# Kernel optimization log

Hardware: AMD Instinct MI355X
Metric: run time of the kernel (lower is better)

The kernel has to match this reference:

```python
import jax, jax.numpy as jnp
import numpy as np

D_MODEL = 128
D_INNER = 256   # expand=2
D_STATE = 16
DT_RANK = 8     # ceil(128/16)
D_CONV = 2
GROUPS = 4
EPS = 1e-5


def _mamba_dir(x, W_in, conv_w, conv_b, W_x, W_dt, b_dt, A_log, D, W_out):
    # x: [B, L, d_model]
    B, L, _ = x.shape
    xz = x @ W_in                               # [B, L, 2*d_inner]
    xp, z = xz[..., :D_INNER], xz[..., D_INNER:]
    # depthwise causal conv, kernel size 2 (pad-left 1)
    xprev = jnp.pad(xp, ((0, 0), (1, 0), (0, 0)))[:, :L]
    xc = jax.nn.silu(xprev * conv_w[:, 0] + xp * conv_w[:, 1] + conv_b)
    xdb = xc @ W_x                              # [B, L, dt_rank + 2*d_state]
    dt_r = xdb[..., :DT_RANK]
    Bc = xdb[..., DT_RANK:DT_RANK + D_STATE]    # [B, L, d_state]
    Cc = xdb[..., DT_RANK + D_STATE:]           # [B, L, d_state]
    dt = jax.nn.softplus(dt_r @ W_dt + b_dt)    # [B, L, d_inner]
    A = -jnp.exp(A_log)                         # [d_inner, d_state]

    def step(h, inp):
        dt_t, B_t, C_t, x_t = inp               # [B,di], [B,ds], [B,ds], [B,di]
        dA = jnp.exp(dt_t[:, :, None] * A)      # [B, di, ds]
        h = dA * h + (dt_t * x_t)[:, :, None] * B_t[:, None, :]
        y = jnp.einsum('bds,bs->bd', h, C_t)
        return h, y

    h0 = jnp.zeros((B, D_INNER, D_STATE), x.dtype)
    xs = (jnp.moveaxis(dt, 1, 0), jnp.moveaxis(Bc, 1, 0),
          jnp.moveaxis(Cc, 1, 0), jnp.moveaxis(xc, 1, 0))
    _, ys = jax.lax.scan(step, h0, xs)          # ys: [L, B, d_inner]
    y = jnp.moveaxis(ys, 0, 1) + D * xc
    y = y * jax.nn.silu(z)
    return y @ W_out                            # [B, L, d_model]


def _groupnorm_silu(x, gamma, beta):
    B, C, H, W = x.shape
    xg = x.reshape(B, GROUPS, C // GROUPS, H, W)
    mu = xg.mean(axis=(2, 3, 4), keepdims=True)
    var = xg.var(axis=(2, 3, 4), keepdims=True)
    xn = ((xg - mu) * jax.lax.rsqrt(var + EPS)).reshape(B, C, H, W)
    return jax.nn.silu(xn * gamma[None, :, None, None] + beta[None, :, None, None])


def setup_inputs() -> dict:
    key = jax.random.key(0)
    ks = jax.random.split(key, 24)
    s = 0.02
    A_log = jnp.log(jnp.tile(jnp.arange(1, D_STATE + 1, dtype=jnp.float32)[None, :], (D_INNER, 1)))
    inp = {"x": jax.random.normal(ks[0], (4, D_MODEL, 64, 64), jnp.float32)}
    for i, sfx in enumerate(("f", "b")):
        o = 1 + 9 * i
        inp[f"W_in_{sfx}"] = jax.random.normal(ks[o], (D_MODEL, 2 * D_INNER)) * s
        inp[f"conv_w_{sfx}"] = jax.random.normal(ks[o + 1], (D_INNER, D_CONV)) * 0.5
        inp[f"conv_b_{sfx}"] = jnp.zeros((D_INNER,))
        inp[f"W_x_{sfx}"] = jax.random.normal(ks[o + 2], (D_INNER, DT_RANK + 2 * D_STATE)) * s
        inp[f"W_dt_{sfx}"] = jax.random.normal(ks[o + 3], (DT_RANK, D_INNER)) * s
        inp[f"b_dt_{sfx}"] = jnp.full((D_INNER,), -3.0)
        inp[f"A_log_{sfx}"] = A_log
        inp[f"D_{sfx}"] = jnp.ones((D_INNER,))
        inp[f"W_out_{sfx}"] = jax.random.normal(ks[o + 4], (D_INNER, D_MODEL)) * s
    inp["gn_gamma"] = jnp.ones((D_MODEL,))
    inp["gn_beta"] = jnp.zeros((D_MODEL,))
    return inp


def reference(x, W_in_f, conv_w_f, conv_b_f, W_x_f, W_dt_f, b_dt_f, A_log_f, D_f, W_out_f,
              W_in_b, conv_w_b, conv_b_b, W_x_b, W_dt_b, b_dt_b, A_log_b, D_b, W_out_b,
              gn_gamma, gn_beta):
    B, C, H, W = x.shape
    xs = x.transpose(0, 2, 3, 1).reshape(B, H * W, C)
    y_f = _mamba_dir(xs, W_in_f, conv_w_f, conv_b_f, W_x_f, W_dt_f, b_dt_f, A_log_f, D_f, W_out_f)
    xr = xs[:, ::-1]
    y_b = _mamba_dir(xr, W_in_b, conv_w_b, conv_b_b, W_x_b, W_dt_b, b_dt_b, A_log_b, D_b, W_out_b)[:, ::-1]
    y = y_f + y_b                               # bidirectional combine
    y = y.reshape(B, H, W, C).transpose(0, 3, 1, 2)
    y = _groupnorm_silu(y, gn_gamma, gn_beta)
    return y + x
```

## Files before the change

kernel.cpp:

```cpp
#include <hip/hip_runtime.h>

#define Bn 4
#define Ln 4096
#define Cn 128
#define DIn 256
#define NCn 128
#define LCn 32
#define ROWS (Bn*Ln)

typedef short s8v __attribute__((ext_vector_type(8)));
typedef short s4v __attribute__((ext_vector_type(4)));
typedef unsigned short u8v __attribute__((ext_vector_type(8)));
typedef unsigned short u4v __attribute__((ext_vector_type(4)));
typedef float f4v __attribute__((ext_vector_type(4)));
typedef float f2v __attribute__((ext_vector_type(2)));

__device__ __forceinline__ float siluf(float x){ return x / (1.f + __expf(-x)); }
__device__ __forceinline__ unsigned short bfr(float f){
  uint u = __float_as_uint(f);
  return (unsigned short)((u + 0x7fffu + ((u>>16)&1u)) >> 16);
}
__device__ __forceinline__ float bf2f(unsigned short u){ return __uint_as_float(((uint)u)<<16); }

__device__ __forceinline__ void sp_w(float r, float& dtv, float& w){
  float e = __expf(-fabsf(r));
  float rc = 1.f / (1.f + e);
  dtv = fmaxf(r, 0.f) + __logf(1.f + e);
  w = (r > 0.f) ? e * rc : rc;
}

__device__ __forceinline__ int tile_off(int r, int gran, int ghalf){
  return ((r>>4)<<9) + ((r&15)<<5) + (((gran ^ ((r>>1)&3)))<<3) + ghalf;
}

#define SMEMB 18432

__global__ __launch_bounds__(256) void k_g1(const float* __restrict__ x,
    const float* __restrict__ Wf, const float* __restrict__ Wb,
    float* __restrict__ xpf, float* __restrict__ xpb,
    unsigned short* __restrict__ zbf, unsigned short* __restrict__ zbb)
{
  const int dir = blockIdx.z;
  const float* __restrict__ W = dir ? Wb : Wf;
  float* __restrict__ xp = dir ? xpb : xpf;
  unsigned short* __restrict__ zb = dir ? zbb : zbf;
  const int row0 = blockIdx.x * 128;
  const int n0 = blockIdx.y;
  const int b = row0 >> 12;
  const int t0 = row0 & (Ln-1);
  const float* __restrict__ xb = x + (size_t)b * Cn * Ln;

  __shared__ __align__(16) char smem[SMEMB];
  short* Ast = (short*)smem;
  short* Bst = (short*)smem + 8*512;
  float* Te  = (float*)smem;

  const int tid = threadIdx.x;
  const int lane = tid & 63;
  const int wid = tid >> 6;
  const int wr = wid >> 1, wc = wid & 1;
  const int r16 = lane & 15, kg = lane >> 4;

  const int q = tid & 31, kq = tid >> 5;
  const int kbase = 4*kq;
  const int g_true = kq >> 1;
  const int ghalf = (kq & 1) * 4;

  f4v acc[4][4];
  #pragma unroll
  for (int i=0;i<4;++i)
    #pragma unroll
    for (int j=0;j<4;++j) acc[i][j] = (f4v){0.f,0.f,0.f,0.f};

  float4 va[4], vb[4];
  {
    #pragma unroll
    for (int kk=0;kk<4;++kk) {
      va[kk] = (dir==0)
        ? *(const float4*)(xb + (size_t)(kbase+kk)*Ln + t0 + 4*q)
        : *(const float4*)(xb + (size_t)(kbase+kk)*Ln + (Ln-4 - t0 - 4*q));
      vb[kk] = *(const float4*)(W + (size_t)(kbase+kk)*512 + n0*128 + 4*q);
    }
  }
  for (int ks=0; ks<4; ++ks) {
    if (ks) __syncthreads();
    #pragma unroll
    for (int e=0;e<4;++e) {
      int r = 4*q + e;
      int off = tile_off(r, g_true, ghalf);
      int c = dir ? (3-e) : e;
      s4v hv;
      #pragma unroll
      for (int kk=0;kk<4;++kk) hv[kk] = (short)bfr(((const float*)&va[kk])[c]);
      *(s4v*)&Ast[off] = hv;
    }
    #pragma unroll
    for (int e=0;e<4;++e) {
      int r = 4*q + e;
      int off = tile_off(r, g_true, ghalf);
      s4v hv;
      #pragma unroll
      for (int kk=0;kk<4;++kk) hv[kk] = (short)bfr(((const float*)&vb[kk])[e]);
      *(s4v*)&Bst[off] = hv;
    }
    __syncthreads();
    if (ks < 3) {
      const int k0n = (ks+1)*32;
      #pragma unroll
      for (int kk=0;kk<4;++kk) {
        va[kk] = (dir==0)
          ? *(const float4*)(xb + (size_t)(k0n+kbase+kk)*Ln + t0 + 4*q)
          : *(const float4*)(xb + (size_t)(k0n+kbase+kk)*Ln + (Ln-4 - t0 - 4*q));
        vb[kk] = *(const float4*)(W + (size_t)(k0n+kbase+kk)*512 + n0*128 + 4*q);
      }
    }
    const int gsh = ((kg ^ ((r16>>1)&3)) << 3);
    s8v fa[4], fb[4];
    #pragma unroll
    for (int m=0;m<4;++m) fa[m] = *(const s8v*)&Ast[(wr*4+m)*512 + r16*32 + gsh];
    #pragma unroll
    for (int n=0;n<4;++n) fb[n] = *(const s8v*)&Bst[(wc*4+n)*512 + r16*32 + gsh];
    #pragma unroll
    for (int m=0;m<4;++m)
      #pragma unroll
      for (int n=0;n<4;++n)
        acc[m][n] = __builtin_amdgcn_mfma_f32_16x16x32_bf16(fa[m], fb[n], acc[m][n], 0,0,0);
  }
  __syncthreads();
  float* Tw = Te + wid*1088;
  #pragma unroll
  for (int m=0;m<4;++m) {
    #pragma unroll
    for (int n=0;n<4;++n)
      #pragma unroll
      for (int v=0;v<4;++v)
        Tw[(kg*4+v)*68 + n*16 + r16] = acc[m][n][v];
    #pragma unroll
    for (int rr=0;rr<4;++rr) {
      int r = rr*4 + (lane>>4);
      int c4 = lane & 15;
      float4 v4 = *(const float4*)&Tw[r*68 + c4*4];
      int row = row0 + wr*64 + m*16 + r;
      int colL = wc*64 + c4*4;
      if (n0 < 2) {
        *(float4*)(xp + (size_t)row*256 + n0*128 + colL) = v4;
      } else {
        u4v u; u[0]=bfr(v4.x); u[1]=bfr(v4.y); u[2]=bfr(v4.z); u[3]=bfr(v4.w);
        *(u4v*)(zb + (size_t)row*256 + (n0-2)*128 + colL) = u;
      }
    }
  }
}

__global__ __launch_bounds__(256) void k_conv(
    const float* __restrict__ xpf, const float* __restrict__ xpb,
    const float* __restrict__ cwf, const float* __restrict__ cwb,
    const float* __restrict__ cbf, const float* __restrict__ cbb,
    unsigned short* __restrict__ xcf, unsigned short* __restrict__ xcb)
{
  const int dir = blockIdx.y;
  const float* __restrict__ xpd = dir ? xpb : xpf;
  const float* __restrict__ cw = dir ? cwb : cwf;
  const float* __restrict__ cb = dir ? cbb : cbf;
  unsigned short* __restrict__ xc = dir ? xcb : xcf;
  const int n4 = ROWS * 64;
  for (int idx4 = blockIdx.x*256 + threadIdx.x; idx4 < n4; idx4 += gridDim.x*256) {
    int row = idx4 >> 6;
    int d0 = (idx4 & 63) * 4;
    float4 cur = *(const float4*)(xpd + (size_t)row*256 + d0);
    float4 prev = make_float4(0.f,0.f,0.f,0.f);
    if (row & (Ln-1)) prev = *(const float4*)(xpd + (size_t)(row-1)*256 + d0);
    float4 cwA = *(const float4*)(cw + d0*2);
    float4 cwB = *(const float4*)(cw + d0*2 + 4);
    float4 cb4 = *(const float4*)(cb + d0);
    u4v r;
    r[0] = bfr(siluf(fmaf(prev.x,cwA.x, fmaf(cur.x,cwA.y, cb4.x))));
    r[1] = bfr(siluf(fmaf(prev.y,cwA.z, fmaf(cur.y,cwA.w, cb4.y))));
    r[2] = bfr(siluf(fmaf(prev.z,cwB.x, fmaf(cur.z,cwB.y, cb4.z))));
    r[3] = bfr(siluf(fmaf(prev.w,cwB.z, fmaf(cur.w,cwB.w, cb4.w))));
    *(u4v*)(xc + (size_t)row*256 + d0) = r;
  }
}

__global__ __launch_bounds__(256) void k_g2(
    const unsigned short* __restrict__ xcf, const unsigned short* __restrict__ xcb,
    const float* __restrict__ Wxf, const float* __restrict__ Wxb,
    float* __restrict__ xdbf, float* __restrict__ xdbb)
{
  const int dir = blockIdx.z;
  const unsigned short* __restrict__ xc = dir ? xcb : xcf;
  const float* __restrict__ Wx = dir ? Wxb : Wxf;
  float* __restrict__ xdb = dir ? xdbb : xdbf;
  const int row0 = blockIdx.x * 64;

  __shared__ __align__(16) short Ast[4*512];
  __shared__ __align__(16) short Bst[4*512];

  const int tid = threadIdx.x;
  const int lane = tid & 63;
  const int wid = tid >> 6;
  const int wr = wid >> 1, wc = wid & 1;
  const int r16 = lane & 15, kg = lane >> 4;
  const int ar = tid >> 2, ag = tid & 3;
  const int bn = tid & 63, bg = tid >> 6;

  f4v acc[2][2];
  #pragma unroll
  for (int i=0;i<2;++i)
    #pragma unroll
    for (int j=0;j<2;++j) acc[i][j] = (f4v){0.f,0.f,0.f,0.f};

  for (int ks=0; ks<8; ++ks) {
    const int k0 = ks*32;
    if (ks) __syncthreads();
    {
      u8v u = *(const u8v*)(xc + (size_t)(row0+ar)*256 + k0 + ag*8);
      *(u8v*)&Ast[tile_off(ar, ag, 0)] = u;
    }
    {
      s8v hv;
      #pragma unroll
      for (int i=0;i<8;++i) {
        int k = k0 + bg*8 + i;
        float f = (bn < 40) ? Wx[(size_t)k*40 + bn] : 0.f;
        hv[i] = (short)bfr(f);
      }
      *(s8v*)&Bst[tile_off(bn, bg, 0)] = hv;
    }
    __syncthreads();
    const int gsh = ((kg ^ ((r16>>1)&3)) << 3);
    s8v fa[2], fb[2];
    #pragma unroll
    for (int m=0;m<2;++m) fa[m] = *(const s8v*)&Ast[(wr*2+m)*512 + r16*32 + gsh];
    #pragma unroll
    for (int n=0;n<2;++n) fb[n] = *(const s8v*)&Bst[(wc*2+n)*512 + r16*32 + gsh];
    #pragma unroll
    for (int m=0;m<2;++m)
      #pragma unroll
      for (int n=0;n<2;++n)
        acc[m][n] = __builtin_amdgcn_mfma_f32_16x16x32_bf16(fa[m], fb[n], acc[m][n], 0,0,0);
  }
  #pragma unroll
  for (int m=0;m<2;++m)
    #pragma unroll
    for (int n=0;n<2;++n) {
      int col = wc*32 + n*16 + r16;
      if (col < 40) {
        #pragma unroll
        for (int v=0;v<4;++v) {
          int row = row0 + wr*32 + m*16 + kg*4 + v;
          xdb[(size_t)row*40 + col] = acc[m][n][v];
        }
      }
    }
}

__global__ __launch_bounds__(128,4) void k_pass1(
    const float* __restrict__ xdbf, const float* __restrict__ xdbb,
    const unsigned short* __restrict__ xcf, const unsigned short* __restrict__ xcb,
    const float* __restrict__ Wdtf, const float* __restrict__ Wdtb,
    const float* __restrict__ bdtf, const float* __restrict__ bdtb,
    const float* __restrict__ Alf, const float* __restrict__ Alb,
    float* __restrict__ sdtf, float* __restrict__ sdtb,
    float* __restrict__ hkf, float* __restrict__ hkb)
{
  const int dir = blockIdx.y;
  const float* __restrict__ xdb = dir ? xdbb : xdbf;
  const unsigned short* __restrict__ xc = dir ? xcb : xcf;
  const float* __restrict__ Wdt = dir ? Wdtb : Wdtf;
  const float* __restrict__ bdt = dir ? bdtb : bdtf;
  const float* __restrict__ Al  = dir ? Alb  : Alf;
  float* __restrict__ sdt = dir ? sdtb : sdtf;
  float* __restrict__ hk  = dir ? hkb  : hkf;
  const int dh = blockIdx.x & 1;
  const int cc = blockIdx.x >> 1;
  const int b = cc >> 7, c = cc & 127;
  const int t0 = c * LCn;
  __shared__ float S[LCn*32];
  const int tid = threadIdx.x;
  #pragma unroll
  for (int j=0;j<6;++j) {
    int idx = tid + j*128;
    int t = idx/24, jj = idx - t*24;
    S[t*32 + jj] = xdb[(size_t)(b*Ln + t0 + t)*40 + jj];
  }
  const int d = dh*128 + tid;
  float Areg[16];
  bool st = true;
  #pragma unroll
  for (int s=0;s<16;++s) {
    Areg[s] = -__expf(Al[d*16+s]);
    st = st && (fabsf(Areg[s] + (float)(s+1)) <= 3e-5f*(float)(s+1));
  }
  f2v wdt2[4];
  #pragma unroll
  for (int j=0;j<4;++j) wdt2[j] = (f2v){Wdt[(2*j)*256+d], Wdt[(2*j+1)*256+d]};
  const float bd = bdt[d];
  f2v h2[8];
  #pragma unroll
  for (int i=0;i<8;++i) h2[i] = (f2v){0.f,0.f};
  float sacc = 0.f;
  const unsigned short* xcp = xc + (size_t)(b*Ln + t0)*256 + d;
  __syncthreads();
  if (st) {
    for (int t=0;t<LCn;++t) {
      float4 sA = *(const float4*)&S[t*32];
      float4 sB = *(const float4*)&S[t*32+4];
      f2v r2 = (f2v){sA.x,sA.y}*wdt2[0] + (f2v){sA.z,sA.w}*wdt2[1];
      r2 = (f2v){sB.x,sB.y}*wdt2[2] + r2;
      r2 = (f2v){sB.z,sB.w}*wdt2[3] + r2;
      float rr = bd + r2.x + r2.y;
      float dtv, wv;
      sp_w(rr, dtv, wv);
      float4 b0 = *(const float4*)&S[t*32+8];
      float4 b1 = *(const float4*)&S[t*32+12];
      float4 b2 = *(const float4*)&S[t*32+16];
      float4 b3 = *(const float4*)&S[t*32+20];
      float xv = bf2f(xcp[(size_t)t*256]);
      float u = dtv * xv;
      sacc += dtv;
      float w2s = wv*wv;
      float w4 = w2s*w2s, w8 = w4*w4;
      f2v wstep = (f2v){w2s, w2s};
      f2v wpa = (f2v){wv, w2s};
      f2v wpb = wpa * (f2v){w8, w8};
      f2v u2 = (f2v){u, u};
      h2[0] = h2[0]*wpa + u2*(f2v){b0.x,b0.y}; wpa *= wstep;
      h2[4] = h2[4]*wpb + u2*(f2v){b2.x,b2.y}; wpb *= wstep;
      h2[1] = h2[1]*wpa + u2*(f2v){b0.z,b0.w}; wpa *= wstep;
      h2[5] = h2[5]*wpb + u2*(f2v){b2.z,b2.w}; wpb *= wstep;
      h2[2] = h2[2]*wpa + u2*(f2v){b1.x,b1.y}; wpa *= wstep;
      h2[6] = h2[6]*wpb + u2*(f2v){b3.x,b3.y}; wpb *= wstep;
      h2[3] = h2[3]*wpa + u2*(f2v){b1.z,b1.w};
      h2[7] = h2[7]*wpb + u2*(f2v){b3.z,b3.w};
    }
  } else {
    for (int t=0;t<LCn;++t) {
      float4 sA = *(const float4*)&S[t*32];
      float4 sB = *(const float4*)&S[t*32+4];
      float rr = bd;
      rr = fmaf(sA.x,wdt2[0].x, fmaf(sA.y,wdt2[0].y, fmaf(sA.z,wdt2[1].x, fmaf(sA.w,wdt2[1].y, rr))));
      rr = fmaf(sB.x,wdt2[2].x, fmaf(sB.y,wdt2[2].y, fmaf(sB.z,wdt2[3].x, fmaf(sB.w,wdt2[3].y, rr))));
      float dtv, wv;
      sp_w(rr, dtv, wv);
      float bq[16];
      #pragma unroll
      for (int i=0;i<4;++i) *(float4*)&bq[4*i] = *(const float4*)&S[t*32 + 8 + 4*i];
      float xv = bf2f(xcp[(size_t)t*256]);
      float u = dtv * xv;
      sacc += dtv;
      #pragma unroll
      for (int s=0;s<16;++s) {
        float hv = (s&1) ? h2[s>>1].y : h2[s>>1].x;
        hv = fmaf(hv, __expf(dtv*Areg[s]), u*bq[s]);
        if (s&1) h2[s>>1].y = hv; else h2[s>>1].x = hv;
      }
    }
  }
  sdt[(size_t)(b*NCn + c)*256 + d] = sacc;
  #pragma unroll
  for (int i=0;i<8;++i) {
    hk[(size_t)((b*NCn + c)*16 + 2*i)*256 + d]   = h2[i].x;
    hk[(size_t)((b*NCn + c)*16 + 2*i+1)*256 + d] = h2[i].y;
  }
}

__global__ __launch_bounds__(256) void k_pass2(
    const float* __restrict__ Alf, const float* __restrict__ Alb,
    const float* __restrict__ sdtf, const float* __restrict__ sdtb,
    float* __restrict__ hkf, float* __restrict__ hkb)
{
  const int dir = blockIdx.y;
  const float* __restrict__ Al  = dir ? Alb : Alf;
  const float* __restrict__ sdt = dir ? sdtb : sdtf;
  float* __restrict__ hk = dir ? hkb : hkf;
  int g = blockIdx.x*256 + threadIdx.x;
  int d = g & 255, s = (g >> 8) & 15, b = g >> 12;
  float Ad = -__expf(Al[d*16+s]);
  float h = 0.f;
  float sd_n = sdt[(size_t)(b*NCn)*256 + d];
  size_t hi_n = (size_t)((b*NCn)*16 + s)*256 + d;
  float he_n = hk[hi_n];
  for (int c=0;c<NCn;++c) {
    float sd = sd_n, he = he_n;
    size_t hi = hi_n;
    if (c+1 < NCn) {
      int bc = b*NCn + c + 1;
      sd_n = sdt[(size_t)bc*256 + d];
      hi_n = (size_t)(bc*16 + s)*256 + d;
      he_n = hk[hi_n];
    }
    hk[hi] = h;
    h = fmaf(__expf(Ad*sd), h, he);
  }
}

__global__ __launch_bounds__(128,4) void k_pass3(
    const float* __restrict__ xdbf, const float* __restrict__ xdbb,
    const unsigned short* __restrict__ xcf, const unsigned short* __restrict__ xcb,
    const float* __restrict__ Wdtf, const float* __restrict__ Wdtb,
    const float* __restrict__ bdtf, const float* __restrict__ bdtb,
    const float* __restrict__ Alf, const float* __restrict__ Alb,
    const float* __restrict__ Dvf, const float* __restrict__ Dvb,
    const float* __restrict__ hkf, const float* __restrict__ hkb,
    const unsigned short* __restrict__ zbf, const unsigned short* __restrict__ zbb,
    unsigned short* __restrict__ ygf, unsigned short* __restrict__ ygb)
{
  const int dir = blockIdx.y;
  const float* __restrict__ xdb = dir ? xdbb : xdbf;
  const unsigned short* __restrict__ xc = dir ? xcb : xcf;
  const float* __restrict__ Wdt = dir ? Wdtb : Wdtf;
  const float* __restrict__ bdt = dir ? bdtb : bdtf;
  const float* __restrict__ Al  = dir ? Alb  : Alf;
  const float* __restrict__ Dv  = dir ? Dvb  : Dvf;
  const float* __restrict__ hk  = dir ? hkb  : hkf;
  const unsigned short* __restrict__ zbd = dir ? zbb : zbf;
  unsigned short* __restrict__ yg = dir ? ygb : ygf;
  const int dh = blockIdx.x & 1;
  const int cc = blockIdx.x >> 1;
  const int b = cc >> 7, c = cc & 127;
  const int t0 = c * LCn;
  __shared__ float S[LCn*48];
  const int tid = threadIdx.x;
  #pragma unroll
  for (int j=0;j<10;++j) {
    int idx = tid + j*128;
    int t = idx/40, jj = idx - t*40;
    S[t*48 + jj] = xdb[(size_t)(b*Ln + t0 + t)*40 + jj];
  }
  const int d = dh*128 + tid;
  float Areg[16];
  bool st = true;
  #pragma unroll
  for (int s=0;s<16;++s) {
    Areg[s] = -__expf(Al[d*16+s]);
    st = st && (fabsf(Areg[s] + (float)(s+1)) <= 3e-5f*(float)(s+1));
  }
  f2v wdt2[4];
  #pragma unroll
  for (int j=0;j<4;++j) wdt2[j] = (f2v){Wdt[(2*j)*256+d], Wdt[(2*j+1)*256+d]};
  const float bd = bdt[d];
  const float Dd = Dv[d];
  f2v h2[8];
  #pragma unroll
  for (int i=0;i<8;++i)
    h2[i] = (f2v){hk[(size_t)((b*NCn + c)*16 + 2*i)*256 + d],
                  hk[(size_t)((b*NCn + c)*16 + 2*i+1)*256 + d]};
  const unsigned short* xcp = xc + (size_t)(b*Ln + t0)*256 + d;
  const unsigned short* zbp = zbd + (size_t)(b*Ln + t0)*256 + d;
  unsigned short* ygp = yg + (size_t)(b*Ln + t0)*256 + d;
  __syncthreads();
  if (st) {
    for (int t=0;t<LCn;++t) {
      float4 sA = *(const float4*)&S[t*48];
      float4 sB = *(const float4*)&S[t*48+4];
      f2v r2 = (f2v){sA.x,sA.y}*wdt2[0] + (f2v){sA.z,sA.w}*wdt2[1];
      r2 = (f2v){sB.x,sB.y}*wdt2[2] + r2;
      r2 = (f2v){sB.z,sB.w}*wdt2[3] + r2;
      float rr = bd + r2.x + r2.y;
      float dtv, wv;
      sp_w(rr, dtv, wv);
      float4 b0 = *(const float4*)&S[t*48+8];
      float4 b1 = *(const float4*)&S[t*48+12];
      float4 b2 = *(const float4*)&S[t*48+16];
      float4 b3 = *(const float4*)&S[t*48+20];
      float4 c0 = *(const float4*)&S[t*48+24];
      float4 c1 = *(const float4*)&S[t*48+28];
      float4 c2 = *(const float4*)&S[t*48+32];
      float4 c3 = *(const float4*)&S[t*48+36];
      float xv = bf2f(xcp[(size_t)t*256]);
      float u = dtv * xv;
      float w2s = wv*wv;
      float w4 = w2s*w2s, w8 = w4*w4;
      f2v wstep = (f2v){w2s, w2s};
      f2v wpa = (f2v){wv, w2s};
      f2v wpb = wpa * (f2v){w8, w8};
      f2v u2 = (f2v){u, u};
      f2v yA = (f2v){0.f,0.f}, yB = (f2v){0.f,0.f};
      h2[0] = h2[0]*wpa + u2*(f2v){b0.x,b0.y}; yA = h2[0]*(f2v){c0.x,c0.y} + yA; wpa *= wstep;
      h2[4] = h2[4]*wpb + u2*(f2v){b2.x,b2.y}; yB = h2[4]*(f2v){c2.x,c2.y} + yB; wpb *= wstep;
      h2[1] = h2[1]*wpa + u2*(f2v){b0.z,b0.w}; yA = h2[1]*(f2v){c0.z,c0.w} + yA; wpa *= wstep;
      h2[5] = h2[5]*wpb + u2*(f2v){b2.z,b2.w}; yB = h2[5]*(f2v){c2.z,c2.w} + yB; wpb *= wstep;
      h2[2] = h2[2]*wpa + u2*(f2v){b1.x,b1.y}; yA = h2[2]*(f2v){c1.x,c1.y} + yA; wpa *= wstep;
      h2[6] = h2[6]*wpb + u2*(f2v){b3.x,b3.y}; yB = h2[6]*(f2v){c3.x,c3.y} + yB; wpb *= wstep;
      h2[3] = h2[3]*wpa + u2*(f2v){b1.z,b1.w}; yA = h2[3]*(f2v){c1.z,c1.w} + yA;
      h2[7] = h2[7]*wpb + u2*(f2v){b3.z,b3.w}; yB = h2[7]*(f2v){c3.z,c3.w} + yB;
      float y = yA.x + yA.y + yB.x + yB.y;
      y = fmaf(Dd, xv, y);
      float zv = bf2f(zbp[(size_t)t*256]);
      ygp[(size_t)t*256] = bfr(y * siluf(zv));
    }
  } else {
    for (int t=0;t<LCn;++t) {
      float4 sA = *(const float4*)&S[t*48];
      float4 sB = *(const float4*)&S[t*48+4];
      float rr = bd;
      rr = fmaf(sA.x,wdt2[0].x, fmaf(sA.y,wdt2[0].y, fmaf(sA.z,wdt2[1].x, fmaf(sA.w,wdt2[1].y, rr))));
      rr = fmaf(sB.x,wdt2[2].x, fmaf(sB.y,wdt2[2].y, fmaf(sB.z,wdt2[3].x, fmaf(sB.w,wdt2[3].y, rr))));
      float dtv, wv;
      sp_w(rr, dtv, wv);
      float bq[16], cq[16];
      #pragma unroll
      for (int i=0;i<4;++i) {
        *(float4*)&bq[4*i] = *(const float4*)&S[t*48 + 8 + 4*i];
        *(float4*)&cq[4*i] = *(const float4*)&S[t*48 + 24 + 4*i];
      }
      float xv = bf2f(xcp[(size_t)t*256]);
      float u = dtv * xv;
      float y = 0.f;
      #pragma unroll
      for (int s=0;s<16;++s) {
        float hv = (s&1) ? h2[s>>1].y : h2[s>>1].x;
        hv = fmaf(hv, __expf(dtv*Areg[s]), u*bq[s]);
        if (s&1) h2[s>>1].y = hv; else h2[s>>1].x = hv;
        y = fmaf(hv, cq[s], y);
      }
      y = fmaf(Dd, xv, y);
      float zv = bf2f(zbp[(size_t)t*256]);
      ygp[(size_t)t*256] = bfr(y * siluf(zv));
    }
  }
}

__global__ __launch_bounds__(256) void k_gout(
    const unsigned short* __restrict__ ygf, const unsigned short* __restrict__ ygb,
    const float* __restrict__ Wof, const float* __restrict__ Wob,
    float* __restrict__ yp)
{
  const int row0 = blockIdx.x * 128;
  const int khalf = blockIdx.y;
  const int dir = blockIdx.z;
  const unsigned short* __restrict__ ygd = dir ? ygb : ygf;
  const float* __restrict__ Wod = dir ? Wob : Wof;
  float* __restrict__ ypart = yp + (size_t)(dir*2 + khalf) * ROWS * 128;
  const int b = row0 >> 12;
  const int l0 = row0 & (Ln-1);

  __shared__ __align__(16) char smem[SMEMB];
  short* Ast = (short*)smem;
  short* Bst = (short*)smem + 8*512;
  float* Te  = (float*)smem;

  const int tid = threadIdx.x;
  const int lane = tid & 63;
  const int wid = tid >> 6;
  const int wr = wid >> 1, wc = wid & 1;
  const int r16 = lane & 15, kg = lane >> 4;

  const int ar = tid >> 1, kh = tid & 1;
  const int q = tid & 31, kq = tid >> 5;
  const int kbase = 4*kq;
  const int g_true = kq >> 1;
  const int ghalf = (kq & 1) * 4;

  f4v acc[4][4];
  #pragma unroll
  for (int i=0;i<4;++i)
    #pragma unroll
    for (int j=0;j<4;++j) acc[i][j] = (f4v){0.f,0.f,0.f,0.f};

  for (int ks=0; ks<4; ++ks) {
    const int kk0 = khalf*128 + ks*32;
    if (ks) __syncthreads();
    {
      int rl = l0 + ar;
      size_t srow = (size_t)b*Ln + (dir ? (Ln-1-rl) : rl);
      const unsigned short* s = ygd + srow*256 + kk0 + kh*16;
      u8v u0 = *(const u8v*)(s);
      u8v u1 = *(const u8v*)(s + 8);
      int o0 = tile_off(ar, 2*kh,   0);
      int o1 = tile_off(ar, 2*kh+1, 0);
      *(u8v*)&Ast[o0] = u0;
      *(u8v*)&Ast[o1] = u1;
    }
    {
      float4 vb[4];
      #pragma unroll
      for (int kk=0;kk<4;++kk)
        vb[kk] = *(const float4*)(Wod + (size_t)(kk0+kbase+kk)*128 + 4*q);
      #pragma unroll
      for (int e=0;e<4;++e) {
        int r = 4*q + e;
        int off = tile_off(r, g_true, ghalf);
        s4v hv;
        #pragma unroll
        for (int kk=0;kk<4;++kk) hv[kk] = (short)bfr(((const float*)&vb[kk])[e]);
        *(s4v*)&Bst[off] = hv;
      }
    }
    __syncthreads();
    const int gsh = ((kg ^ ((r16>>1)&3)) << 3);
    s8v fa[4], fb[4];
    #pragma unroll
    for (int m=0;m<4;++m) fa[m] = *(const s8v*)&Ast[(wr*4+m)*512 + r16*32 + gsh];
    #pragma unroll
    for (int n=0;n<4;++n) fb[n] = *(const s8v*)&Bst[(wc*4+n)*512 + r16*32 + gsh];
    #pragma unroll
    for (int m=0;m<4;++m)
      #pragma unroll
      for (int n=0;n<4;++n)
        acc[m][n] = __builtin_amdgcn_mfma_f32_16x16x32_bf16(fa[m], fb[n], acc[m][n], 0,0,0);
  }
  __syncthreads();
  float* Tw = Te + wid*1088;
  #pragma unroll
  for (int m=0;m<4;++m) {
    #pragma unroll
    for (int n=0;n<4;++n)
      #pragma unroll
      for (int v=0;v<4;++v)
        Tw[(kg*4+v)*68 + n*16 + r16] = acc[m][n][v];
    #pragma unroll
    for (int rr=0;rr<4;++rr) {
      int r = rr*4 + (lane>>4);
      int c4 = lane & 15;
      float4 v4 = *(const float4*)&Tw[r*68 + c4*4];
      int row = row0 + wr*64 + m*16 + r;
      *(float4*)(ypart + (size_t)row*128 + wc*64 + c4*4) = v4;
    }
  }
}

__global__ __launch_bounds__(256) void k_gnstat(const float* __restrict__ yp,
    float* __restrict__ ysum, float* __restrict__ part)
{
  const int bg = blockIdx.x >> 4;
  const int blk = blockIdx.x & 15;
  const int b = bg >> 2, g = bg & 3;
  const size_t P = (size_t)ROWS*128;
  float s=0.f, q=0.f;
  #pragma unroll
  for (int i=0;i<8;++i) {
    int e4 = blk*2048 + threadIdx.x + i*256;
    int l = e4 >> 3, c4 = e4 & 7;
    size_t base = (size_t)(b*Ln + l)*128 + g*32 + c4*4;
    float4 v0 = *(const float4*)(yp + base);
    float4 v1 = *(const float4*)(yp + P + base);
    float4 v2 = *(const float4*)(yp + 2*P + base);
    float4 v3 = *(const float4*)(yp + 3*P + base);
    float4 v;
    v.x = v0.x+v1.x+v2.x+v3.x;
    v.y = v0.y+v1.y+v2.y+v3.y;
    v.z = v0.z+v1.z+v2.z+v3.z;
    v.w = v0.w+v1.w+v2.w+v3.w;
    *(float4*)(ysum + base) = v;
    s += v.x+v.y+v.z+v.w;
    q = fmaf(v.x,v.x, fmaf(v.y,v.y, fmaf(v.z,v.z, fmaf(v.w,v.w, q))));
  }
  __shared__ float rs[256], rq[256];
  rs[threadIdx.x]=s; rq[threadIdx.x]=q;
  __syncthreads();
  for (int off=128; off>0; off>>=1) {
    if (threadIdx.x < off) { rs[threadIdx.x]+=rs[threadIdx.x+off]; rq[threadIdx.x]+=rq[threadIdx.x+off]; }
    __syncthreads();
  }
  if (threadIdx.x==0) { part[blockIdx.x*2]=rs[0]; part[blockIdx.x*2+1]=rq[0]; }
}

__global__ void k_gnred(const float* __restrict__ part, float* __restrict__ mr)
{
  int t = threadIdx.x;
  if (t < 16) {
    float s=0.f,q=0.f;
    for (int k=0;k<16;++k){ s+=part[(t*16+k)*2]; q+=part[(t*16+k)*2+1]; }
    const float inv = 1.f/131072.f;
    float mean = s*inv;
    float var = fmaf(-mean, mean, q*inv);
    mr[t*2] = mean;
    mr[t*2+1] = rsqrtf(var + 1e-5f);
  }
}

__global__ __launch_bounds__(256) void k_gnapply(const float* __restrict__ ysum,
    const float* __restrict__ mr, const float* __restrict__ gamma, const float* __restrict__ beta,
    const float* __restrict__ x, float* __restrict__ out)
{
  const int b = blockIdx.x >> 6;
  const int l0 = (blockIdx.x & 63) * 64;
  __shared__ float T[64][132];
  const int tid = threadIdx.x;
  #pragma unroll
  for (int j=0;j<8;++j) {
    int f = tid + j*256;
    int l = f >> 5, c4 = f & 31;
    *(float4*)&T[l][c4*4] = *(const float4*)(ysum + (size_t)(b*Ln + l0 + l)*128 + c4*4);
  }
  __syncthreads();
  #pragma unroll
  for (int j=0;j<8;++j) {
    int f = tid + j*256;
    int c = f >> 4, lv = f & 15;
    int bg = b*4 + (c>>5);
    float mean = mr[bg*2];
    float rstd = mr[bg*2+1];
    float gam = gamma[c], bet = beta[c];
    size_t base = (size_t)(b*Cn + c)*Ln + l0 + lv*4;
    float4 xv = *(const float4*)(x + base);
    float4 r;
    r.x = siluf(fmaf((T[lv*4+0][c]-mean)*rstd, gam, bet)) + xv.x;
    r.y = siluf(fmaf((T[lv*4+1][c]-mean)*rstd, gam, bet)) + xv.y;
    r.z = siluf(fmaf((T[lv*4+2][c]-mean)*rstd, gam, bet)) + xv.z;
    r.w = siluf(fmaf((T[lv*4+3][c]-mean)*rstd, gam, bet)) + xv.w;
    *(float4*)(out + base) = r;
  }
}

extern "C" void kernel_launch(void* const* d_in, const int* in_sizes, int n_in,
                              void* d_out, int out_size, void* d_ws, size_t ws_size,
                              hipStream_t stream) {
  const float* x      = (const float*)d_in[0];
  const float* W_in_f = (const float*)d_in[1];
  const float* cw_f   = (const float*)d_in[2];
  const float* cb_f   = (const float*)d_in[3];
  const float* Wx_f   = (const float*)d_in[4];
  const float* Wdt_f  = (const float*)d_in[5];
  const float* bdt_f  = (const float*)d_in[6];
  const float* Al_f   = (const float*)d_in[7];
  const float* D_f    = (const float*)d_in[8];
  const float* Wo_f   = (const float*)d_in[9];
  const float* W_in_b = (const float*)d_in[10];
  const float* cw_b   = (const float*)d_in[11];
  const float* cb_b   = (const float*)d_in[12];
  const float* Wx_b   = (const float*)d_in[13];
  const float* Wdt_b  = (const float*)d_in[14];
  const float* bdt_b  = (const float*)d_in[15];
  const float* Al_b   = (const float*)d_in[16];
  const float* D_b    = (const float*)d_in[17];
  const float* Wo_b   = (const float*)d_in[18];
  const float* gamma  = (const float*)d_in[19];
  const float* beta   = (const float*)d_in[20];
  float* out = (float*)d_out;

  float* w = (float*)d_ws;
  size_t o = 0;
  float* xp0 = w + o; o += (size_t)ROWS*256;
  float* xp1 = w + o; o += (size_t)ROWS*256;
  unsigned short* xc0 = (unsigned short*)(w + o); o += (size_t)ROWS*128;
  unsigned short* xc1 = (unsigned short*)(w + o); o += (size_t)ROWS*128;
  unsigned short* zb0 = (unsigned short*)(w + o); o += (size_t)ROWS*128;
  unsigned short* zb1 = (unsigned short*)(w + o); o += (size_t)ROWS*128;
  unsigned short* yg0 = (unsigned short*)(w + o); o += (size_t)ROWS*128;
  unsigned short* yg1 = (unsigned short*)(w + o); o += (size_t)ROWS*128;
  float* xdb0 = w + o; o += (size_t)ROWS*40;
  float* xdb1 = w + o; o += (size_t)ROWS*40;
  float* sdt0 = w + o; o += (size_t)Bn*NCn*256;
  float* sdt1 = w + o; o += (size_t)Bn*NCn*256;
  float* hk0  = w + o; o += (size_t)Bn*NCn*16*256;
  float* hk1  = w + o; o += (size_t)Bn*NCn*16*256;
  float* part = w + o; o += 512;
  float* mr   = w + o; o += 32;
  float* yp   = xp0;
  float* ysum = xdb0;
  if (ws_size < o*sizeof(float)) return;

  k_g1<<<dim3(ROWS/128, 4, 2), 256, 0, stream>>>(x, W_in_f, W_in_b, xp0, xp1, zb0, zb1);
  k_conv<<<dim3(1024, 2), 256, 0, stream>>>(xp0, xp1, cw_f, cw_b, cb_f, cb_b, xc0, xc1);
  k_g2<<<dim3(ROWS/64, 1, 2), 256, 0, stream>>>(xc0, xc1, Wx_f, Wx_b, xdb0, xdb1);
  k_pass1<<<dim3(Bn*NCn*2, 2), 128, 0, stream>>>(xdb0, xdb1, xc0, xc1, Wdt_f, Wdt_b,
                                                 bdt_f, bdt_b, Al_f, Al_b, sdt0, sdt1, hk0, hk1);
  k_pass2<<<dim3(64, 2), 256, 0, stream>>>(Al_f, Al_b, sdt0, sdt1, hk0, hk1);
  k_pass3<<<dim3(Bn*NCn*2, 2), 128, 0, stream>>>(xdb0, xdb1, xc0, xc1, Wdt_f, Wdt_b,
                                                 bdt_f, bdt_b, Al_f, Al_b, D_f, D_b,
                                                 hk0, hk1, zb0, zb1, yg0, yg1);
  k_gout<<<dim3(ROWS/128, 2, 2), 256, 0, stream>>>(yg0, yg1, Wo_f, Wo_b, yp);
  k_gnstat<<<dim3(256), 256, 0, stream>>>(yp, ysum, part);
  k_gnred<<<dim3(1), 64, 0, stream>>>(part, mr);
  k_gnapply<<<dim3(256), 256, 0, stream>>>(ysum, mr, gamma, beta, x, out);
}
```

Baseline: 148.5 us.

## Compute zero-init chunk output in pass1 and apply state correction in pass3

```diff
diff --git a/kernel.cpp b/kernel.cpp
--- a/kernel.cpp
+++ b/kernel.cpp
@@ -261,8 +261,10 @@
     const float* __restrict__ Wdtf, const float* __restrict__ Wdtb,
     const float* __restrict__ bdtf, const float* __restrict__ bdtb,
     const float* __restrict__ Alf, const float* __restrict__ Alb,
+    const float* __restrict__ Dvf, const float* __restrict__ Dvb,
     float* __restrict__ sdtf, float* __restrict__ sdtb,
-    float* __restrict__ hkf, float* __restrict__ hkb)
+    float* __restrict__ hkf, float* __restrict__ hkb,
+    unsigned int* __restrict__ dtwf, unsigned int* __restrict__ dtwb)
 {
   const int dir = blockIdx.y;
   const float* __restrict__ xdb = dir ? xdbb : xdbf;
@@ -270,19 +272,21 @@
   const float* __restrict__ Wdt = dir ? Wdtb : Wdtf;
   const float* __restrict__ bdt = dir ? bdtb : bdtf;
   const float* __restrict__ Al  = dir ? Alb  : Alf;
+  const float* __restrict__ Dv  = dir ? Dvb  : Dvf;
   float* __restrict__ sdt = dir ? sdtb : sdtf;
   float* __restrict__ hk  = dir ? hkb  : hkf;
+  unsigned int* __restrict__ dtw = dir ? dtwb : dtwf;
   const int dh = blockIdx.x & 1;
   const int cc = blockIdx.x >> 1;
   const int b = cc >> 7, c = cc & 127;
   const int t0 = c * LCn;
-  __shared__ float S[LCn*32];
+  __shared__ float S[LCn*48];
   const int tid = threadIdx.x;
   #pragma unroll
-  for (int j=0;j<6;++j) {
+  for (int j=0;j<10;++j) {
     int idx = tid + j*128;
-    int t = idx/24, jj = idx - t*24;
-    S[t*32 + jj] = xdb[(size_t)(b*Ln + t0 + t)*40 + jj];
+    int t = idx/40, jj = idx - t*40;
+    S[t*48 + jj] = xdb[(size_t)(b*Ln + t0 + t)*40 + jj];
   }
   const int d = dh*128 + tid;
   float Areg[16];
@@ -296,26 +300,33 @@
   #pragma unroll
   for (int j=0;j<4;++j) wdt2[j] = (f2v){Wdt[(2*j)*256+d], Wdt[(2*j+1)*256+d]};
   const float bd = bdt[d];
+  const float Dd = Dv[d];
   f2v h2[8];
   #pragma unroll
   for (int i=0;i<8;++i) h2[i] = (f2v){0.f,0.f};
   float sacc = 0.f;
   const unsigned short* xcp = xc + (size_t)(b*Ln + t0)*256 + d;
+  unsigned int* dtwp = dtw + (size_t)(b*Ln + t0)*256 + d;
   __syncthreads();
   if (st) {
+    float Wc = 1.f;
     for (int t=0;t<LCn;++t) {
-      float4 sA = *(const float4*)&S[t*32];
-      float4 sB = *(const float4*)&S[t*32+4];
+      float4 sA = *(const float4*)&S[t*48];
+      float4 sB = *(const float4*)&S[t*48+4];
       f2v r2 = (f2v){sA.x,sA.y}*wdt2[0] + (f2v){sA.z,sA.w}*wdt2[1];
       r2 = (f2v){sB.x,sB.y}*wdt2[2] + r2;
       r2 = (f2v){sB.z,sB.w}*wdt2[3] + r2;
       float rr = bd + r2.x + r2.y;
       float dtv, wv;
       sp_w(rr, dtv, wv);
-      float4 b0 = *(const float4*)&S[t*32+8];
-      float4 b1 = *(const float4*)&S[t*32+12];
-      float4 b2 = *(const float4*)&S[t*32+16];
-      float4 b3 = *(const float4*)&S[t*32+20];
+      float4 b0 = *(const float4*)&S[t*48+8];
+      float4 b1 = *(const float4*)&S[t*48+12];
+      float4 b2 = *(const float4*)&S[t*48+16];
+      float4 b3 = *(const float4*)&S[t*48+20];
+      float4 c0 = *(const float4*)&S[t*48+24];
+      float4 c1 = *(const float4*)&S[t*48+28];
+      float4 c2 = *(const float4*)&S[t*48+32];
+      float4 c3 = *(const float4*)&S[t*48+36];
       float xv = bf2f(xcp[(size_t)t*256]);
       float u = dtv * xv;
       sacc += dtv;
@@ -325,36 +336,53 @@
       f2v wpa = (f2v){wv, w2s};
       f2v wpb = wpa * (f2v){w8, w8};
       f2v u2 = (f2v){u, u};
-      h2[0] = h2[0]*wpa + u2*(f2v){b0.x,b0.y}; wpa *= wstep;
-      h2[4] = h2[4]*wpb + u2*(f2v){b2.x,b2.y}; wpb *= wstep;
-      h2[1] = h2[1]*wpa + u2*(f2v){b0.z,b0.w}; wpa *= wstep;
-      h2[5] = h2[5]*wpb + u2*(f2v){b2.z,b2.w}; wpb *= wstep;
-      h2[2] = h2[2]*wpa + u2*(f2v){b1.x,b1.y}; wpa *= wstep;
-      h2[6] = h2[6]*wpb + u2*(f2v){b3.x,b3.y}; wpb *= wstep;
-      h2[3] = h2[3]*wpa + u2*(f2v){b1.z,b1.w};
-      h2[7] = h2[7]*wpb + u2*(f2v){b3.z,b3.w};
+      f2v yA = (f2v){0.f,0.f}, yB = (f2v){0.f,0.f};
+      h2[0] = h2[0]*wpa + u2*(f2v){b0.x,b0.y}; yA = h2[0]*(f2v){c0.x,c0.y} + yA; wpa *= wstep;
+      h2[4] = h2[4]*wpb + u2*(f2v){b2.x,b2.y}; yB = h2[4]*(f2v){c2.x,c2.y} + yB; wpb *= wstep;
+      h2[1] = h2[1]*wpa + u2*(f2v){b0.z,b0.w}; yA = h2[1]*(f2v){c0.z,c0.w} + yA; wpa *= wstep;
+      h2[5] = h2[5]*wpb + u2*(f2v){b2.z,b2.w}; yB = h2[5]*(f2v){c2.z,c2.w} + yB; wpb *= wstep;
+      h2[2] = h2[2]*wpa + u2*(f2v){b1.x,b1.y}; yA = h2[2]*(f2v){c1.x,c1.y} + yA; wpa *= wstep;
+      h2[6] = h2[6]*wpb + u2*(f2v){b3.x,b3.y}; yB = h2[6]*(f2v){c3.x,c3.y} + yB; wpb *= wstep;
+      h2[3] = h2[3]*wpa + u2*(f2v){b1.z,b1.w}; yA = h2[3]*(f2v){c1.z,c1.w} + yA;
+      h2[7] = h2[7]*wpb + u2*(f2v){b3.z,b3.w}; yB = h2[7]*(f2v){c3.z,c3.w} + yB;
+      float y = yA.x + yA.y + yB.x + yB.y;
+      y = fmaf(Dd, xv, y);
+      Wc *= wv;
+      unsigned int pk = ((unsigned int)bfr(y) << 16)
+                      | (unsigned int)(unsigned short)fminf(Wc*65536.f, 65535.f);
+      dtwp[(size_t)t*256] = pk;
     }
   } else {
+    float Dt = 0.f;
     for (int t=0;t<LCn;++t) {
-      float4 sA = *(const float4*)&S[t*32];
-      float4 sB = *(const float4*)&S[t*32+4];
+      float4 sA = *(const float4*)&S[t*48];
+      float4 sB = *(const float4*)&S[t*48+4];
       float rr = bd;
       rr = fmaf(sA.x,wdt2[0].x, fmaf(sA.y,wdt2[0].y, fmaf(sA.z,wdt2[1].x, fmaf(sA.w,wdt2[1].y, rr))));
       rr = fmaf(sB.x,wdt2[2].x, fmaf(sB.y,wdt2[2].y, fmaf(sB.z,wdt2[3].x, fmaf(sB.w,wdt2[3].y, rr))));
       float dtv, wv;
       sp_w(rr, dtv, wv);
-      float bq[16];
-      #pragma unroll
-      for (int i=0;i<4;++i) *(float4*)&bq[4*i] = *(const float4*)&S[t*32 + 8 + 4*i];
+      float bq[16], cq[16];
+      #pragma unroll
+      for (int i=0;i<4;++i) {
+        *(float4*)&bq[4*i] = *(const float4*)&S[t*48 + 8 + 4*i];
+        *(float4*)&cq[4*i] = *(const float4*)&S[t*48 + 24 + 4*i];
+      }
       float xv = bf2f(xcp[(size_t)t*256]);
       float u = dtv * xv;
       sacc += dtv;
+      Dt += dtv;
+      float y = 0.f;
       #pragma unroll
       for (int s=0;s<16;++s) {
         float hv = (s&1) ? h2[s>>1].y : h2[s>>1].x;
         hv = fmaf(hv, __expf(dtv*Areg[s]), u*bq[s]);
         if (s&1) h2[s>>1].y = hv; else h2[s>>1].x = hv;
+        y = fmaf(hv, cq[s], y);
       }
+      y = fmaf(Dd, xv, y);
+      unsigned int pk = ((unsigned int)bfr(y) << 16) | (unsigned int)bfr(Dt);
+      dtwp[(size_t)t*256] = pk;
     }
   }
   sdt[(size_t)(b*NCn + c)*256 + d] = sacc;
@@ -395,24 +423,18 @@
   }
 }
 
-__global__ __launch_bounds__(128,4) void k_pass3(
+__global__ __launch_bounds__(128,4) void k_passC(
     const float* __restrict__ xdbf, const float* __restrict__ xdbb,
-    const unsigned short* __restrict__ xcf, const unsigned short* __restrict__ xcb,
-    const float* __restrict__ Wdtf, const float* __restrict__ Wdtb,
-    const float* __restrict__ bdtf, const float* __restrict__ bdtb,
+    const unsigned int* __restrict__ dtwf, const unsigned int* __restrict__ dtwb,
     const float* __restrict__ Alf, const float* __restrict__ Alb,
-    const float* __restrict__ Dvf, const float* __restrict__ Dvb,
     const float* __restrict__ hkf, const float* __restrict__ hkb,
     const unsigned short* __restrict__ zbf, const unsigned short* __restrict__ zbb,
     unsigned short* __restrict__ ygf, unsigned short* __restrict__ ygb)
 {
   const int dir = blockIdx.y;
   const float* __restrict__ xdb = dir ? xdbb : xdbf;
-  const unsigned short* __restrict__ xc = dir ? xcb : xcf;
-  const float* __restrict__ Wdt = dir ? Wdtb : Wdtf;
-  const float* __restrict__ bdt = dir ? bdtb : bdtf;
+  const unsigned int* __restrict__ dtw = dir ? dtwb : dtwf;
   const float* __restrict__ Al  = dir ? Alb  : Alf;
-  const float* __restrict__ Dv  = dir ? Dvb  : Dvf;
   const float* __restrict__ hk  = dir ? hkb  : hkf;
   const unsigned short* __restrict__ zbd = dir ? zbb : zbf;
   unsigned short* __restrict__ yg = dir ? ygb : ygf;
@@ -420,13 +442,13 @@
   const int cc = blockIdx.x >> 1;
   const int b = cc >> 7, c = cc & 127;
   const int t0 = c * LCn;
-  __shared__ float S[LCn*48];
+  __shared__ float S[LCn*16];
   const int tid = threadIdx.x;
   #pragma unroll
-  for (int j=0;j<10;++j) {
+  for (int j=0;j<4;++j) {
     int idx = tid + j*128;
-    int t = idx/40, jj = idx - t*40;
-    S[t*48 + jj] = xdb[(size_t)(b*Ln + t0 + t)*40 + jj];
+    int t = idx >> 4, jj = idx & 15;
+    S[idx] = xdb[(size_t)(b*Ln + t0 + t)*40 + 24 + jj];
   }
   const int d = dh*128 + tid;
   float Areg[16];
@@ -436,86 +458,54 @@
     Areg[s] = -__expf(Al[d*16+s]);
     st = st && (fabsf(Areg[s] + (float)(s+1)) <= 3e-5f*(float)(s+1));
   }
-  f2v wdt2[4];
-  #pragma unroll
-  for (int j=0;j<4;++j) wdt2[j] = (f2v){Wdt[(2*j)*256+d], Wdt[(2*j+1)*256+d]};
-  const float bd = bdt[d];
-  const float Dd = Dv[d];
-  f2v h2[8];
+  f2v hin2[8];
   #pragma unroll
   for (int i=0;i<8;++i)
-    h2[i] = (f2v){hk[(size_t)((b*NCn + c)*16 + 2*i)*256 + d],
-                  hk[(size_t)((b*NCn + c)*16 + 2*i+1)*256 + d]};
-  const unsigned short* xcp = xc + (size_t)(b*Ln + t0)*256 + d;
+    hin2[i] = (f2v){hk[(size_t)((b*NCn + c)*16 + 2*i)*256 + d],
+                    hk[(size_t)((b*NCn + c)*16 + 2*i+1)*256 + d]};
+  const unsigned int* dtwp = dtw + (size_t)(b*Ln + t0)*256 + d;
   const unsigned short* zbp = zbd + (size_t)(b*Ln + t0)*256 + d;
   unsigned short* ygp = yg + (size_t)(b*Ln + t0)*256 + d;
   __syncthreads();
   if (st) {
+    #pragma unroll 4
     for (int t=0;t<LCn;++t) {
-      float4 sA = *(const float4*)&S[t*48];
-      float4 sB = *(const float4*)&S[t*48+4];
-      f2v r2 = (f2v){sA.x,sA.y}*wdt2[0] + (f2v){sA.z,sA.w}*wdt2[1];
-      r2 = (f2v){sB.x,sB.y}*wdt2[2] + r2;
-      r2 = (f2v){sB.z,sB.w}*wdt2[3] + r2;
-      float rr = bd + r2.x + r2.y;
-      float dtv, wv;
-      sp_w(rr, dtv, wv);
-      float4 b0 = *(const float4*)&S[t*48+8];
-      float4 b1 = *(const float4*)&S[t*48+12];
-      float4 b2 = *(const float4*)&S[t*48+16];
-      float4 b3 = *(const float4*)&S[t*48+20];
-      float4 c0 = *(const float4*)&S[t*48+24];
-      float4 c1 = *(const float4*)&S[t*48+28];
-      float4 c2 = *(const float4*)&S[t*48+32];
-      float4 c3 = *(const float4*)&S[t*48+36];
-      float xv = bf2f(xcp[(size_t)t*256]);
-      float u = dtv * xv;
-      float w2s = wv*wv;
-      float w4 = w2s*w2s, w8 = w4*w4;
-      f2v wstep = (f2v){w2s, w2s};
-      f2v wpa = (f2v){wv, w2s};
-      f2v wpb = wpa * (f2v){w8, w8};
-      f2v u2 = (f2v){u, u};
-      f2v yA = (f2v){0.f,0.f}, yB = (f2v){0.f,0.f};
-      h2[0] = h2[0]*wpa + u2*(f2v){b0.x,b0.y}; yA = h2[0]*(f2v){c0.x,c0.y} + yA; wpa *= wstep;
-      h2[4] = h2[4]*wpb + u2*(f2v){b2.x,b2.y}; yB = h2[4]*(f2v){c2.x,c2.y} + yB; wpb *= wstep;
-      h2[1] = h2[1]*wpa + u2*(f2v){b0.z,b0.w}; yA = h2[1]*(f2v){c0.z,c0.w} + yA; wpa *= wstep;
-      h2[5] = h2[5]*wpb + u2*(f2v){b2.z,b2.w}; yB = h2[5]*(f2v){c2.z,c2.w} + yB; wpb *= wstep;
-      h2[2] = h2[2]*wpa + u2*(f2v){b1.x,b1.y}; yA = h2[2]*(f2v){c1.x,c1.y} + yA; wpa *= wstep;
-      h2[6] = h2[6]*wpb + u2*(f2v){b3.x,b3.y}; yB = h2[6]*(f2v){c3.x,c3.y} + yB; wpb *= wstep;
-      h2[3] = h2[3]*wpa + u2*(f2v){b1.z,b1.w}; yA = h2[3]*(f2v){c1.z,c1.w} + yA;
-      h2[7] = h2[7]*wpb + u2*(f2v){b3.z,b3.w}; yB = h2[7]*(f2v){c3.z,c3.w} + yB;
-      float y = yA.x + yA.y + yB.x + yB.y;
-      y = fmaf(Dd, xv, y);
+      unsigned int pw = dtwp[(size_t)t*256];
+      float yv = bf2f((unsigned short)(pw >> 16));
+      float Wc = (float)(pw & 0xffffu) * (1.f/65536.f);
+      float4 c0 = *(const float4*)&S[t*16];
+      float4 c1 = *(const float4*)&S[t*16+4];
+      float4 c2 = *(const float4*)&S[t*16+8];
+      float4 c3 = *(const float4*)&S[t*16+12];
+      float Wc2 = Wc*Wc;
+      float Wc4 = Wc2*Wc2, Wc8 = Wc4*Wc4;
+      f2v wstep = (f2v){Wc2, Wc2};
+      f2v wpa = (f2v){Wc, Wc2};
+      f2v wpb = wpa * (f2v){Wc8, Wc8};
+      f2v corr = (f2v){0.f,0.f};
+      corr = (hin2[0]*wpa)*(f2v){c0.x,c0.y} + corr; wpa *= wstep;
+      corr = (hin2[4]*wpb)*(f2v){c2.x,c2.y} + corr; wpb *= wstep;
+      corr = (hin2[1]*wpa)*(f2v){c0.z,c0.w} + corr; wpa *= wstep;
+      corr = (hin2[5]*wpb)*(f2v){c2.z,c2.w} + corr; wpb *= wstep;
+      corr = (hin2[2]*wpa)*(f2v){c1.x,c1.y} + corr; wpa *= wstep;
+      corr = (hin2[6]*wpb)*(f2v){c3.x,c3.y} + corr; wpb *= wstep;
+      corr = (hin2[3]*wpa)*(f2v){c1.z,c1.w} + corr;
+      corr = (hin2[7]*wpb)*(f2v){c3.z,c3.w} + corr;
+      float y = yv + corr.x + corr.y;
       float zv = bf2f(zbp[(size_t)t*256]);
       ygp[(size_t)t*256] = bfr(y * siluf(zv));
     }
   } else {
     for (int t=0;t<LCn;++t) {
-      float4 sA = *(const float4*)&S[t*48];
-      float4 sB = *(const float4*)&S[t*48+4];
-      float rr = bd;
-      rr = fmaf(sA.x,wdt2[0].x, fmaf(sA.y,wdt2[0].y, fmaf(sA.z,wdt2[1].x, fmaf(sA.w,wdt2[1].y, rr))));
-      rr = fmaf(sB.x,wdt2[2].x, fmaf(sB.y,wdt2[2].y, fmaf(sB.z,wdt2[3].x, fmaf(sB.w,wdt2[3].y, rr))));
-      float dtv, wv;
-      sp_w(rr, dtv, wv);
-      float bq[16], cq[16];
-      #pragma unroll
-      for (int i=0;i<4;++i) {
-        *(float4*)&bq[4*i] = *(const float4*)&S[t*48 + 8 + 4*i];
-        *(float4*)&cq[4*i] = *(const float4*)&S[t*48 + 24 + 4*i];
+      unsigned int pw = dtwp[(size_t)t*256];
+      float yv = bf2f((unsigned short)(pw >> 16));
+      float Dt = bf2f((unsigned short)(pw & 0xffffu));
+      float y = yv;
+      #pragma unroll
+      for (int s=0;s<16;++s) {
+        float hv = (s&1) ? hin2[s>>1].y : hin2[s>>1].x;
+        y = fmaf(S[t*16+s], __expf(Areg[s]*Dt)*hv, y);
       }
-      float xv = bf2f(xcp[(size_t)t*256]);
-      float u = dtv * xv;
-      float y = 0.f;
-      #pragma unroll
-      for (int s=0;s<16;++s) {
-        float hv = (s&1) ? h2[s>>1].y : h2[s>>1].x;
-        hv = fmaf(hv, __expf(dtv*Areg[s]), u*bq[s]);
-        if (s&1) h2[s>>1].y = hv; else h2[s>>1].x = hv;
-        y = fmaf(hv, cq[s], y);
-      }
-      y = fmaf(Dd, xv, y);
       float zv = bf2f(zbp[(size_t)t*256]);
       ygp[(size_t)t*256] = bfr(y * siluf(zv));
     }
@@ -749,6 +739,8 @@
   float* hk1  = w + o; o += (size_t)Bn*NCn*16*256;
   float* part = w + o; o += 512;
   float* mr   = w + o; o += 32;
+  unsigned int* dtw0 = (unsigned int*)xp0;
+  unsigned int* dtw1 = (unsigned int*)xp1;
   float* yp   = xp0;
   float* ysum = xdb0;
   if (ws_size < o*sizeof(float)) return;
@@ -757,10 +749,10 @@
   k_conv<<<dim3(1024, 2), 256, 0, stream>>>(xp0, xp1, cw_f, cw_b, cb_f, cb_b, xc0, xc1);
   k_g2<<<dim3(ROWS/64, 1, 2), 256, 0, stream>>>(xc0, xc1, Wx_f, Wx_b, xdb0, xdb1);
   k_pass1<<<dim3(Bn*NCn*2, 2), 128, 0, stream>>>(xdb0, xdb1, xc0, xc1, Wdt_f, Wdt_b,
-                                                 bdt_f, bdt_b, Al_f, Al_b, sdt0, sdt1, hk0, hk1);
+                                                 bdt_f, bdt_b, Al_f, Al_b, D_f, D_b,
+                                                 sdt0, sdt1, hk0, hk1, dtw0, dtw1);
   k_pass2<<<dim3(64, 2), 256, 0, stream>>>(Al_f, Al_b, sdt0, sdt1, hk0, hk1);
-  k_pass3<<<dim3(Bn*NCn*2, 2), 128, 0, stream>>>(xdb0, xdb1, xc0, xc1, Wdt_f, Wdt_b,
-                                                 bdt_f, bdt_b, Al_f, Al_b, D_f, D_b,
+  k_passC<<<dim3(Bn*NCn*2, 2), 128, 0, stream>>>(xdb0, xdb1, dtw0, dtw1, Al_f, Al_b,
                                                  hk0, hk1, zb0, zb1, yg0, yg1);
   k_gout<<<dim3(ROWS/128, 2, 2), 256, 0, stream>>>(yg0, yg1, Wo_f, Wo_b, yp);
   k_gnstat<<<dim3(256), 256, 0, stream>>>(yp, ysum, part);
```

After: 154.5 us. 1.04x slower.
